# Kernel tuning notes

Measured on AMD Instinct MI355X. Metric: run time of the kernel, lower is better.

Reference implementation:

```python
import jax, jax.numpy as jnp
import numpy as np

E = 1408      # hidden_size
H = 16        # num heads
D = E // H    # head_dim = 88
S = 1025      # (448/14)^2 + 1 cls token
B = 8


def setup_inputs() -> dict:
    key = jax.random.key(0)
    ks = jax.random.split(key, 11)
    scale = 1.0 / np.sqrt(E)
    inp = {
        "hidden_states": jax.random.normal(ks[0], (B, S, E), dtype=jnp.float32),
    }
    # rotary freqs as cos/sin of random angles, shape (S, D//2)
    theta = jax.random.uniform(ks[1], (S, D // 2), dtype=jnp.float32) * (2.0 * np.pi)
    inp["freqs_cos"] = jnp.cos(theta)
    inp["freqs_sin"] = jnp.sin(theta)
    # projection weights stored torch-style: (out_features, in_features)
    inp["q_w"] = jax.random.normal(ks[2], (E, E), dtype=jnp.float32) * scale
    inp["q_b"] = jax.random.normal(ks[3], (E,), dtype=jnp.float32) * scale
    inp["k_w"] = jax.random.normal(ks[4], (E, E), dtype=jnp.float32) * scale
    inp["k_b"] = jax.random.normal(ks[5], (E,), dtype=jnp.float32) * scale
    inp["v_w"] = jax.random.normal(ks[6], (E, E), dtype=jnp.float32) * scale
    inp["v_b"] = jax.random.normal(ks[7], (E,), dtype=jnp.float32) * scale
    inp["o_w"] = jax.random.normal(ks[8], (E, E), dtype=jnp.float32) * scale
    inp["o_b"] = jax.random.normal(ks[9], (E,), dtype=jnp.float32) * scale
    return inp


def _apply_rope(x, cos, sin):
    # x: (B, S, H, D); interpret last dim as D//2 complex pairs (re, im)
    xr = x.astype(jnp.float32).reshape(*x.shape[:-1], D // 2, 2)
    re, im = xr[..., 0], xr[..., 1]
    c = cos[None, :, None, :]  # broadcast over batch and heads
    s = sin[None, :, None, :]
    out_re = re * c - im * s
    out_im = re * s + im * c
    return jnp.stack([out_re, out_im], axis=-1).reshape(x.shape).astype(x.dtype)


def reference(hidden_states, freqs_cos, freqs_sin, q_w, q_b, k_w, k_b, v_w, v_b, o_w, o_b):
    b, s, _ = hidden_states.shape
    q = (hidden_states @ q_w.T + q_b).reshape(b, s, H, D)
    k = (hidden_states @ k_w.T + k_b).reshape(b, s, H, D)
    v = (hidden_states @ v_w.T + v_b).reshape(b, s, H, D)
    q = _apply_rope(q, freqs_cos, freqs_sin)
    k = _apply_rope(k, freqs_cos, freqs_sin)
    # (B, H, S, D)
    q = q.transpose(0, 2, 1, 3)
    k = k.transpose(0, 2, 1, 3)
    v = v.transpose(0, 2, 1, 3)
    scores = jnp.einsum('bhqd,bhkd->bhqk', q, k) / np.sqrt(D)
    attn = jax.nn.softmax(scores.astype(jnp.float32), axis=-1).astype(q.dtype)
    out = jnp.einsum('bhqk,bhkd->bqhd', attn, v).reshape(b, s, H * D)
    out = out @ o_w.T + o_b
    return out, attn
```

## Files before the change

kernel.cpp:

```cpp
#include <hip/hip_runtime.h>

typedef unsigned short u16;
typedef __attribute__((ext_vector_type(8))) short short8;
typedef __attribute__((ext_vector_type(4))) float f32x4;
typedef __attribute__((ext_vector_type(16))) float f32x16;

#define E_DIM 1408
#define H_HEADS 16
#define S_SEQ 1025
#define B_BATCH 8
#define S_PAD 1088
#define D_PAD 128
#define M_ROWS 8200
#define M_PAD 8320

struct __attribute__((packed, aligned(4))) f4u { float x, y, z, w; };

__device__ __forceinline__ u16 f2bf(float f){
  union { float f; unsigned u; } x; x.f = f;
  unsigned r = x.u + 0x7fffu + ((x.u >> 16) & 1u);
  return (u16)(r >> 16);
}

__device__ __forceinline__ void gload16(const void* g, void* l){
  __builtin_amdgcn_global_load_lds(
      (const __attribute__((address_space(1))) void*)g,
      (__attribute__((address_space(3))) void*)l, 16, 0, 0);
}

__device__ __forceinline__ f32x4 mfma16(short8 a, short8 b, f32x4 c){
  return __builtin_amdgcn_mfma_f32_16x16x32_bf16(a, b, c, 0, 0, 0);
}
__device__ __forceinline__ f32x16 mfma32(short8 a, short8 b, f32x16 c){
  return __builtin_amdgcn_mfma_f32_32x32x16_bf16(a, b, c, 0, 0, 0);
}

__global__ __launch_bounds__(256) void cvt_kernel(const float* __restrict__ src,
                                                  u16* __restrict__ dst, int n8){
  int i = blockIdx.x * 256 + threadIdx.x;
  if (i >= n8) return;
  const float4* s4 = (const float4*)src;
  float4 a = s4[2*i], b = s4[2*i+1];
  union { u16 u[8]; short8 v; } o;
  o.u[0]=f2bf(a.x); o.u[1]=f2bf(a.y); o.u[2]=f2bf(a.z); o.u[3]=f2bf(a.w);
  o.u[4]=f2bf(b.x); o.u[5]=f2bf(b.y); o.u[6]=f2bf(b.z); o.u[7]=f2bf(b.w);
  ((short8*)dst)[i] = o.v;
}

__global__ __launch_bounds__(256) void zero_pads_kernel(u16* __restrict__ Q,
                                                        u16* __restrict__ K,
                                                        u16* __restrict__ Vt){
  int i = blockIdx.x * 256 + threadIdx.x;
  const int n1 = 128 * S_PAD * 8;
  const int n2 = 128 * 63 * 96;
  const int n3 = 128 * 96 * 63;
  if (i < n1){
    int d = 88 + (i & 7); int t = i >> 3;
    int s = t % S_PAD; int bh = t / S_PAD;
    size_t o = ((size_t)bh * S_PAD + s) * D_PAD + d;
    Q[o] = 0; K[o] = 0;
  } else if (i < n1 + n2){
    int j = i - n1;
    int d = j % 96; int t = j / 96;
    int s = 1025 + t % 63; int bh = t / 63;
    size_t o = ((size_t)bh * S_PAD + s) * D_PAD + d;
    Q[o] = 0; K[o] = 0;
  } else if (i < n1 + n2 + n3){
    int j = i - n1 - n2;
    int d = j % 96; int t = j / 96;
    int sp = 1025 + t % 63; int bh = t / 63;
    Vt[((size_t)bh * D_PAD + d) * S_PAD + sp] = 0;
  }
}

template<int MODE>
__global__ __launch_bounds__(256) void gemm_bt(
    const u16* __restrict__ A, const u16* __restrict__ W,
    const float* __restrict__ b_q, const float* __restrict__ b_k,
    const float* __restrict__ b_v,
    u16* __restrict__ Qb, u16* __restrict__ Kb, u16* __restrict__ Vtb,
    float* __restrict__ outF,
    const float* __restrict__ fcos, const float* __restrict__ fsin)
{
  __shared__ u16 As[128*32];
  __shared__ u16 Bs[128*32];
  const int tid = threadIdx.x;
  const int lane = tid & 63, wid = tid >> 6;
  const int cl = lane & 15, grp = lane >> 4;
  const int n0 = blockIdx.x * 128, m0 = blockIdx.y * 128;
  const int region = (MODE == 0) ? (blockIdx.x / 11) : 0;
  const int wm = (wid >> 1) * 64, wn = (wid & 1) * 64;
  f32x4 acc[4][4] = {};

  for (int k0 = 0; k0 < E_DIM; k0 += 32){
    __syncthreads();
#pragma unroll
    for (int rd = 0; rd < 2; ++rd){
      int G = rd * 256 + tid;
      int row = G >> 2, cg = G & 3;
      gload16(A + (size_t)(m0 + row) * E_DIM + k0 + cg * 8, (char*)As + (size_t)G * 16);
      gload16(W + (size_t)(n0 + row) * E_DIM + k0 + cg * 8, (char*)Bs + (size_t)G * 16);
    }
    __syncthreads();
    short8 av[4], bv[4];
#pragma unroll
    for (int i = 0; i < 4; ++i) av[i] = *(const short8*)&As[(wm + i*16 + cl)*32 + grp*8];
#pragma unroll
    for (int j = 0; j < 4; ++j) bv[j] = *(const short8*)&Bs[(wn + j*16 + cl)*32 + grp*8];
#pragma unroll
    for (int i = 0; i < 4; ++i)
#pragma unroll
      for (int j = 0; j < 4; ++j)
        acc[i][j] = mfma16(av[i], bv[j], acc[i][j]);
  }

  const float* bias = (MODE == 1) ? b_q : (region == 0 ? b_q : (region == 1 ? b_k : b_v));

#pragma unroll
  for (int i = 0; i < 4; ++i){
#pragma unroll
    for (int j = 0; j < 4; ++j){
      const int jcol = n0 + wn + j*16 + cl;
      const int jl = jcol - region * E_DIM;
      const float bsv = bias[jl];
      const int hh = jl / 88;
      const int dd = jl - hh * 88;
#pragma unroll
      for (int r = 0; r < 4; ++r){
        const int rrow = m0 + wm + i*16 + grp*4 + r;
        float v = acc[i][j][r] + bsv;
        if (MODE == 0 && region <= 1){
          float other = __shfl_xor(v, 1);
          int bb = rrow / 1025;
          int spos = rrow - bb * 1025;
          int pp = dd >> 1;
          float c = fcos[spos * 44 + pp];
          float s = fsin[spos * 44 + pp];
          float o = fmaf(v, c, (jl & 1) ? (other * s) : -(other * s));
          if (rrow < M_ROWS){
            size_t dst = (((size_t)(bb * 16 + hh)) * S_PAD + spos) * D_PAD + dd;
            (region ? Kb : Qb)[dst] = f2bf(o);
          }
        } else if (MODE == 0){
          if (rrow < M_ROWS){
            int bb = rrow / 1025;
            int spos = rrow - bb * 1025;
            size_t dst = (((size_t)(bb * 16 + hh)) * D_PAD + dd) * S_PAD + spos;
            Vtb[dst] = f2bf(v);
          }
        } else {
          if (rrow < M_ROWS) outF[(size_t)rrow * E_DIM + jcol] = v;
        }
      }
    }
  }
}

#define STAGE_K(buf, kt)                                                        \
  {                                                                             \
    _Pragma("unroll")                                                           \
    for (int rd = 0; rd < 2; ++rd){                                             \
      int G = rd * 512 + tid;                                                   \
      int row = G >> 4, c = G & 15;                                             \
      gload16(Kg + (size_t)((kt) * 64 + row) * 128 + ((c ^ (row & 15)) * 8),    \
              (char*)&Ks[buf][0] + (size_t)G * 16);                             \
    }                                                                           \
  }

#define STAGE_V(buf, kt)                                                        \
  {                                                                             \
    { int G = tid; int row = G >> 3, c = G & 7;                                 \
      gload16(Vg + (size_t)row * S_PAD + (kt) * 64 + ((c ^ (row & 7)) * 8),     \
              (char*)&Vs[buf][0] + (size_t)G * 16); }                           \
    if (tid < 256){                                                             \
      int G = 512 + tid; int row = G >> 3, c = G & 7;                           \
      gload16(Vg + (size_t)row * S_PAD + (kt) * 64 + ((c ^ (row & 7)) * 8),     \
              (char*)&Vs[buf][0] + (size_t)G * 16); }                           \
  }

__global__ __launch_bounds__(512) void attn_kernel(
    const u16* __restrict__ Qb, const u16* __restrict__ Kb,
    const u16* __restrict__ Vtb, float* __restrict__ attn,
    u16* __restrict__ AO)
{
  __shared__ u16 Ks[2][64 * 128];
  __shared__ u16 Vs[2][96 * 64];
  const int tid = threadIdx.x, wid = tid >> 6, lane = tid & 63;
  const int q5 = lane & 31, hi = lane >> 5;
  int lin = blockIdx.x + gridDim.x * blockIdx.y;
  lin = (lin & 7) * 80 + (lin >> 3);
  const int qt = lin % 5, bh = lin / 5;
  const int b = bh >> 4, h = bh & 15;
  const u16* __restrict__ Qg = Qb + (size_t)bh * S_PAD * 128;
  const u16* __restrict__ Kg = Kb + (size_t)bh * S_PAD * 128;
  const u16* __restrict__ Vg = Vtb + (size_t)bh * 128 * S_PAD;
  const int qrow = qt * 256 + wid * 32 + q5;
  const int qrowc = (qrow < S_PAD) ? qrow : (S_PAD - 1);
  const float SCALE = 0.10660035817780521f;

  short8 qf[6];
#pragma unroll
  for (int ds = 0; ds < 6; ++ds)
    qf[ds] = *(const short8*)&Qg[(size_t)qrowc * 128 + ds * 16 + hi * 8];

  float l_run = 0.f;
  STAGE_K(0, 0);
  __syncthreads();
  for (int kt = 0; kt < 17; ++kt){
    const int cur = kt & 1;
    if (kt < 16) STAGE_K(cur ^ 1, kt + 1);
#pragma unroll
    for (int ks = 0; ks < 2; ++ks){
      f32x16 sc = {};
      const int krow = ks * 32 + q5;
#pragma unroll
      for (int ds = 0; ds < 6; ++ds){
        int c = ds * 2 + hi;
        short8 kf = *(const short8*)&Ks[cur][krow * 128 + ((c ^ (krow & 15)) * 8)];
        sc = mfma32(kf, qf[ds], sc);
      }
      if (kt == 16){
#pragma unroll
        for (int r = 0; r < 16; ++r){
          int kabs = 1024 + ks * 32 + (r & 3) + 8 * (r >> 2) + 4 * hi;
          l_run += (kabs < 1025) ? __expf(sc[r] * SCALE) : 0.f;
        }
      } else {
#pragma unroll
        for (int r = 0; r < 16; ++r) l_run += __expf(sc[r] * SCALE);
      }
    }
    __syncthreads();
  }
  l_run += __shfl_xor(l_run, 32);
  const float linv = 1.0f / l_run;

  f32x16 oacc[3] = {};
  STAGE_K(0, 0);
  STAGE_V(0, 0);
  __syncthreads();
  for (int kt = 0; kt < 17; ++kt){
    const int cur = kt & 1;
    if (kt < 16){ STAGE_K(cur ^ 1, kt + 1); STAGE_V(cur ^ 1, kt + 1); }
#pragma unroll
    for (int ks = 0; ks < 2; ++ks){
      f32x16 sc = {};
      const int krow = ks * 32 + q5;
#pragma unroll
      for (int ds = 0; ds < 6; ++ds){
        int c = ds * 2 + hi;
        short8 kf = *(const short8*)&Ks[cur][krow * 128 + ((c ^ (krow & 15)) * 8)];
        sc = mfma32(kf, qf[ds], sc);
      }
#pragma unroll
      for (int r = 0; r < 16; ++r) sc[r] = __expf(sc[r] * SCALE) * linv;

      if (qrow < 1025){
        if (kt < 16){
          float* arow = attn + ((size_t)bh * 1025 + qrow) * 1025 + kt * 64 + ks * 32 + 4 * hi;
#pragma unroll
          for (int g = 0; g < 4; ++g){
            f4u w4 = { sc[4*g], sc[4*g+1], sc[4*g+2], sc[4*g+3] };
            *(f4u*)(arow + 8 * g) = w4;
          }
        } else {
#pragma unroll
          for (int r = 0; r < 16; ++r){
            int kabs = 1024 + ks * 32 + (r & 3) + 8 * (r >> 2) + 4 * hi;
            if (kabs < 1025)
              attn[((size_t)bh * 1025 + qrow) * 1025 + kabs] = sc[r];
          }
        }
      }

      unsigned w[8], sx[8];
#pragma unroll
      for (int j = 0; j < 8; ++j)
        w[j] = (unsigned)f2bf(sc[2*j]) | ((unsigned)f2bf(sc[2*j+1]) << 16);
#pragma unroll
      for (int j = 0; j < 8; ++j) sx[j] = __shfl_xor(w[j], 32);
      union U { unsigned u[4]; short8 s8; } a0, a1;
      a0.u[0] = hi ? sx[2] : w[0];
      a0.u[1] = hi ? sx[3] : w[1];
      a0.u[2] = hi ? w[2]  : sx[0];
      a0.u[3] = hi ? w[3]  : sx[1];
      a1.u[0] = hi ? sx[6] : w[4];
      a1.u[1] = hi ? sx[7] : w[5];
      a1.u[2] = hi ? w[6]  : sx[4];
      a1.u[3] = hi ? w[7]  : sx[5];

#pragma unroll
      for (int dt = 0; dt < 3; ++dt){
        const int vrow = dt * 32 + q5;
        int c0 = ks * 4 + hi;
        short8 vf0 = *(const short8*)&Vs[cur][vrow * 64 + ((c0 ^ (vrow & 7)) * 8)];
        oacc[dt] = mfma32(a0.s8, vf0, oacc[dt]);
        int c1 = ks * 4 + 2 + hi;
        short8 vf1 = *(const short8*)&Vs[cur][vrow * 64 + ((c1 ^ (vrow & 7)) * 8)];
        oacc[dt] = mfma32(a1.s8, vf1, oacc[dt]);
      }
    }
    __syncthreads();
  }

  const int qb0 = qt * 256 + wid * 32;
#pragma unroll
  for (int dt = 0; dt < 3; ++dt){
    const int d = dt * 32 + q5;
    if (d < 88){
#pragma unroll
      for (int r = 0; r < 16; ++r){
        int qq = qb0 + (r & 3) + 8 * (r >> 2) + 4 * hi;
        if (qq < 1025)
          AO[((size_t)b * 1025 + qq) * E_DIM + h * 88 + d] = f2bf(oacc[dt][r]);
      }
    }
  }
}

extern "C" void kernel_launch(void* const* d_in, const int* in_sizes, int n_in,
                              void* d_out, int out_size, void* d_ws, size_t ws_size,
                              hipStream_t stream)
{
  const float* hs   = (const float*)d_in[0];
  const float* fcos = (const float*)d_in[1];
  const float* fsin = (const float*)d_in[2];
  const float* q_w  = (const float*)d_in[3];
  const float* q_b  = (const float*)d_in[4];
  const float* k_w  = (const float*)d_in[5];
  const float* k_b  = (const float*)d_in[6];
  const float* v_w  = (const float*)d_in[7];
  const float* v_b  = (const float*)d_in[8];
  const float* o_w  = (const float*)d_in[9];
  const float* o_b  = (const float*)d_in[10];
  float* out0 = (float*)d_out;
  float* attn = out0 + (size_t)B_BATCH * S_SEQ * E_DIM;

  char* ws = (char*)d_ws;
  size_t off = 0;
  auto take = [&](size_t bytes){
    char* p = ws + off; off += (bytes + 255) & ~(size_t)255; return p;
  };
  u16* Xb  = (u16*)take((size_t)M_PAD * E_DIM * 2);
  u16* Wb  = (u16*)take((size_t)4 * E_DIM * E_DIM * 2);
  u16* Qb  = (u16*)take((size_t)128 * S_PAD * D_PAD * 2);
  u16* Kb  = (u16*)take((size_t)128 * S_PAD * D_PAD * 2);
  u16* Vtb = (u16*)take((size_t)128 * D_PAD * S_PAD * 2);
  u16* AO  = (u16*)take((size_t)M_PAD * E_DIM * 2);

  cvt_kernel<<<(1443200 + 255) / 256, 256, 0, stream>>>(hs, Xb, 1443200);
  cvt_kernel<<<968, 256, 0, stream>>>(q_w, Wb + 0 * (size_t)E_DIM * E_DIM, 247808);
  cvt_kernel<<<968, 256, 0, stream>>>(k_w, Wb + 1 * (size_t)E_DIM * E_DIM, 247808);
  cvt_kernel<<<968, 256, 0, stream>>>(v_w, Wb + 2 * (size_t)E_DIM * E_DIM, 247808);
  cvt_kernel<<<968, 256, 0, stream>>>(o_w, Wb + 3 * (size_t)E_DIM * E_DIM, 247808);
  zero_pads_kernel<<<10400, 256, 0, stream>>>(Qb, Kb, Vtb);

  gemm_bt<0><<<dim3(33, 65), 256, 0, stream>>>(Xb, Wb, q_b, k_b, v_b,
                                               Qb, Kb, Vtb, nullptr, fcos, fsin);

  attn_kernel<<<dim3(5, 128), 512, 0, stream>>>(Qb, Kb, Vtb, attn, AO);

  gemm_bt<1><<<dim3(11, 65), 256, 0, stream>>>(AO, Wb + 3 * (size_t)E_DIM * E_DIM,
                                               o_b, o_b, o_b,
                                               nullptr, nullptr, nullptr, out0, fcos, fsin);
}
```

Baseline: 587.2 us.

## Restructure attention tiling, fold softmax scale into Q, batch weight conversions

Several changes land at once. The softmax scale times log2(e) is folded into Q inside the QKV GEMM epilogue, so attention can use exp2 directly and apply the normaliser as a log subtraction. The attention kernel moves to 128-query blocks with 256 threads and a single V buffer, and uses cvt_pk_bf16 plus permlane32_swap for the P repack. The GEMM gets an XCD-aware block remap and s_setprio around its MFMAs, and the four weight conversions are merged into one launch. The padded-key correction subtracts a constant 63 (exp2(0) for each zero-padded key) instead of masking, which relies on padded K being exactly zero, and the single V buffer adds a synchronisation per tile.

```diff
diff --git a/kernel.cpp b/kernel.cpp
--- a/kernel.cpp
+++ b/kernel.cpp
@@ -33,6 +33,15 @@
 }
 __device__ __forceinline__ f32x16 mfma32(short8 a, short8 b, f32x16 c){
   return __builtin_amdgcn_mfma_f32_32x32x16_bf16(a, b, c, 0, 0, 0);
+}
+
+__device__ __forceinline__ unsigned cvtpk(float a, float b){
+  unsigned r;
+  asm("v_cvt_pk_bf16_f32 %0, %1, %2" : "=v"(r) : "v"(a), "v"(b));
+  return r;
+}
+__device__ __forceinline__ void plswap(unsigned &a, unsigned &b){
+  asm("v_permlane32_swap_b32 %0, %1" : "+v"(a), "+v"(b));
 }
 
 __global__ __launch_bounds__(256) void cvt_kernel(const float* __restrict__ src,
@@ -45,6 +54,24 @@
   o.u[0]=f2bf(a.x); o.u[1]=f2bf(a.y); o.u[2]=f2bf(a.z); o.u[3]=f2bf(a.w);
   o.u[4]=f2bf(b.x); o.u[5]=f2bf(b.y); o.u[6]=f2bf(b.z); o.u[7]=f2bf(b.w);
   ((short8*)dst)[i] = o.v;
+}
+
+__global__ __launch_bounds__(256) void cvt4_kernel(const float* __restrict__ s0,
+                                                   const float* __restrict__ s1,
+                                                   const float* __restrict__ s2,
+                                                   const float* __restrict__ s3,
+                                                   u16* __restrict__ dst, int n8){
+  int i = blockIdx.x * 256 + threadIdx.x;
+  if (i >= n8) return;
+  const float* src = (blockIdx.y == 0) ? s0 : (blockIdx.y == 1) ? s1
+                   : (blockIdx.y == 2) ? s2 : s3;
+  u16* d = dst + (size_t)blockIdx.y * n8 * 8;
+  const float4* s4 = (const float4*)src;
+  float4 a = s4[2*i], b = s4[2*i+1];
+  union { u16 u[8]; short8 v; } o;
+  o.u[0]=f2bf(a.x); o.u[1]=f2bf(a.y); o.u[2]=f2bf(a.z); o.u[3]=f2bf(a.w);
+  o.u[4]=f2bf(b.x); o.u[5]=f2bf(b.y); o.u[6]=f2bf(b.z); o.u[7]=f2bf(b.w);
+  ((short8*)d)[i] = o.v;
 }
 
 __global__ __launch_bounds__(256) void zero_pads_kernel(u16* __restrict__ Q,
@@ -87,8 +114,16 @@
   const int tid = threadIdx.x;
   const int lane = tid & 63, wid = tid >> 6;
   const int cl = lane & 15, grp = lane >> 4;
-  const int n0 = blockIdx.x * 128, m0 = blockIdx.y * 128;
-  const int region = (MODE == 0) ? (blockIdx.x / 11) : 0;
+
+  const int nwg = (int)(gridDim.x * gridDim.y);
+  const int orig = blockIdx.x + gridDim.x * blockIdx.y;
+  const int qq = nwg >> 3, rr = nwg & 7;
+  const int xcd = orig & 7, kk = orig >> 3;
+  const int wg = (xcd < rr ? xcd * (qq + 1) : rr * (qq + 1) + (xcd - rr) * qq) + kk;
+  const int bx = wg % (int)gridDim.x, by = wg / (int)gridDim.x;
+
+  const int n0 = bx * 128, m0 = by * 128;
+  const int region = (MODE == 0) ? (bx / 11) : 0;
   const int wm = (wid >> 1) * 64, wn = (wid & 1) * 64;
   f32x4 acc[4][4] = {};
 
@@ -107,14 +142,17 @@
     for (int i = 0; i < 4; ++i) av[i] = *(const short8*)&As[(wm + i*16 + cl)*32 + grp*8];
 #pragma unroll
     for (int j = 0; j < 4; ++j) bv[j] = *(const short8*)&Bs[(wn + j*16 + cl)*32 + grp*8];
+    __builtin_amdgcn_s_setprio(1);
 #pragma unroll
     for (int i = 0; i < 4; ++i)
 #pragma unroll
       for (int j = 0; j < 4; ++j)
         acc[i][j] = mfma16(av[i], bv[j], acc[i][j]);
+    __builtin_amdgcn_s_setprio(0);
   }
 
   const float* bias = (MODE == 1) ? b_q : (region == 0 ? b_q : (region == 1 ? b_k : b_v));
+  const float QSCALE = 0.15379181f;
 
 #pragma unroll
   for (int i = 0; i < 4; ++i){
@@ -137,6 +175,7 @@
           float c = fcos[spos * 44 + pp];
           float s = fsin[spos * 44 + pp];
           float o = fmaf(v, c, (jl & 1) ? (other * s) : -(other * s));
+          if (region == 0) o *= QSCALE;
           if (rrow < M_ROWS){
             size_t dst = (((size_t)(bb * 16 + hh)) * S_PAD + spos) * D_PAD + dd;
             (region ? Kb : Qb)[dst] = f2bf(o);
@@ -159,51 +198,50 @@
 #define STAGE_K(buf, kt)                                                        \
   {                                                                             \
     _Pragma("unroll")                                                           \
-    for (int rd = 0; rd < 2; ++rd){                                             \
-      int G = rd * 512 + tid;                                                   \
+    for (int rd = 0; rd < 4; ++rd){                                             \
+      int G = rd * 256 + tid;                                                   \
       int row = G >> 4, c = G & 15;                                             \
       gload16(Kg + (size_t)((kt) * 64 + row) * 128 + ((c ^ (row & 15)) * 8),    \
               (char*)&Ks[buf][0] + (size_t)G * 16);                             \
     }                                                                           \
   }
 
-#define STAGE_V(buf, kt)                                                        \
+#define STAGE_V(kt)                                                             \
   {                                                                             \
-    { int G = tid; int row = G >> 3, c = G & 7;                                 \
+    _Pragma("unroll")                                                           \
+    for (int rd = 0; rd < 3; ++rd){                                             \
+      int G = rd * 256 + tid;                                                   \
+      int row = G >> 3, c = G & 7;                                              \
       gload16(Vg + (size_t)row * S_PAD + (kt) * 64 + ((c ^ (row & 7)) * 8),     \
-              (char*)&Vs[buf][0] + (size_t)G * 16); }                           \
-    if (tid < 256){                                                             \
-      int G = 512 + tid; int row = G >> 3, c = G & 7;                           \
-      gload16(Vg + (size_t)row * S_PAD + (kt) * 64 + ((c ^ (row & 7)) * 8),     \
-              (char*)&Vs[buf][0] + (size_t)G * 16); }                           \
-  }
-
-__global__ __launch_bounds__(512) void attn_kernel(
+              (char*)Vs + (size_t)G * 16);                                      \
+    }                                                                           \
+  }
+
+__global__ __launch_bounds__(256, 3) void attn_kernel(
     const u16* __restrict__ Qb, const u16* __restrict__ Kb,
     const u16* __restrict__ Vtb, float* __restrict__ attn,
     u16* __restrict__ AO)
 {
   __shared__ u16 Ks[2][64 * 128];
-  __shared__ u16 Vs[2][96 * 64];
+  __shared__ u16 Vs[96 * 64];
   const int tid = threadIdx.x, wid = tid >> 6, lane = tid & 63;
   const int q5 = lane & 31, hi = lane >> 5;
   int lin = blockIdx.x + gridDim.x * blockIdx.y;
-  lin = (lin & 7) * 80 + (lin >> 3);
-  const int qt = lin % 5, bh = lin / 5;
+  lin = (lin & 7) * 144 + (lin >> 3);
+  const int qt = lin % 9, bh = lin / 9;
   const int b = bh >> 4, h = bh & 15;
   const u16* __restrict__ Qg = Qb + (size_t)bh * S_PAD * 128;
   const u16* __restrict__ Kg = Kb + (size_t)bh * S_PAD * 128;
   const u16* __restrict__ Vg = Vtb + (size_t)bh * 128 * S_PAD;
-  const int qrow = qt * 256 + wid * 32 + q5;
+  const int qrow = qt * 128 + wid * 32 + q5;
   const int qrowc = (qrow < S_PAD) ? qrow : (S_PAD - 1);
-  const float SCALE = 0.10660035817780521f;
 
   short8 qf[6];
 #pragma unroll
   for (int ds = 0; ds < 6; ++ds)
     qf[ds] = *(const short8*)&Qg[(size_t)qrowc * 128 + ds * 16 + hi * 8];
 
-  float l_run = 0.f;
+  float l0 = 0.f, l1 = 0.f, l2 = 0.f, l3 = 0.f;
   STAGE_K(0, 0);
   __syncthreads();
   for (int kt = 0; kt < 17; ++kt){
@@ -213,47 +251,51 @@
     for (int ks = 0; ks < 2; ++ks){
       f32x16 sc = {};
       const int krow = ks * 32 + q5;
+      __builtin_amdgcn_s_setprio(1);
 #pragma unroll
       for (int ds = 0; ds < 6; ++ds){
         int c = ds * 2 + hi;
         short8 kf = *(const short8*)&Ks[cur][krow * 128 + ((c ^ (krow & 15)) * 8)];
         sc = mfma32(kf, qf[ds], sc);
       }
-      if (kt == 16){
-#pragma unroll
-        for (int r = 0; r < 16; ++r){
-          int kabs = 1024 + ks * 32 + (r & 3) + 8 * (r >> 2) + 4 * hi;
-          l_run += (kabs < 1025) ? __expf(sc[r] * SCALE) : 0.f;
-        }
-      } else {
-#pragma unroll
-        for (int r = 0; r < 16; ++r) l_run += __expf(sc[r] * SCALE);
+      __builtin_amdgcn_s_setprio(0);
+#pragma unroll
+      for (int r = 0; r < 16; r += 4){
+        l0 += __builtin_amdgcn_exp2f(sc[r]);
+        l1 += __builtin_amdgcn_exp2f(sc[r+1]);
+        l2 += __builtin_amdgcn_exp2f(sc[r+2]);
+        l3 += __builtin_amdgcn_exp2f(sc[r+3]);
       }
     }
     __syncthreads();
   }
-  l_run += __shfl_xor(l_run, 32);
-  const float linv = 1.0f / l_run;
+  float l = (l0 + l1) + (l2 + l3);
+  l += __shfl_xor(l, 32);
+  l -= 63.0f;
+  const float lg2l = __builtin_amdgcn_logf(l);
 
   f32x16 oacc[3] = {};
   STAGE_K(0, 0);
-  STAGE_V(0, 0);
+  STAGE_V(0);
   __syncthreads();
   for (int kt = 0; kt < 17; ++kt){
     const int cur = kt & 1;
-    if (kt < 16){ STAGE_K(cur ^ 1, kt + 1); STAGE_V(cur ^ 1, kt + 1); }
+    if (kt < 16) STAGE_K(cur ^ 1, kt + 1);
+    short8 pa0[2], pa1[2];
 #pragma unroll
     for (int ks = 0; ks < 2; ++ks){
       f32x16 sc = {};
       const int krow = ks * 32 + q5;
+      __builtin_amdgcn_s_setprio(1);
 #pragma unroll
       for (int ds = 0; ds < 6; ++ds){
         int c = ds * 2 + hi;
         short8 kf = *(const short8*)&Ks[cur][krow * 128 + ((c ^ (krow & 15)) * 8)];
         sc = mfma32(kf, qf[ds], sc);
       }
-#pragma unroll
-      for (int r = 0; r < 16; ++r) sc[r] = __expf(sc[r] * SCALE) * linv;
+      __builtin_amdgcn_s_setprio(0);
+#pragma unroll
+      for (int r = 0; r < 16; ++r) sc[r] = __builtin_amdgcn_exp2f(sc[r] - lg2l);
 
       if (qrow < 1025){
         if (kt < 16){
@@ -273,46 +315,47 @@
         }
       }
 
-      unsigned w[8], sx[8];
-#pragma unroll
-      for (int j = 0; j < 8; ++j)
-        w[j] = (unsigned)f2bf(sc[2*j]) | ((unsigned)f2bf(sc[2*j+1]) << 16);
-#pragma unroll
-      for (int j = 0; j < 8; ++j) sx[j] = __shfl_xor(w[j], 32);
-      union U { unsigned u[4]; short8 s8; } a0, a1;
-      a0.u[0] = hi ? sx[2] : w[0];
-      a0.u[1] = hi ? sx[3] : w[1];
-      a0.u[2] = hi ? w[2]  : sx[0];
-      a0.u[3] = hi ? w[3]  : sx[1];
-      a1.u[0] = hi ? sx[6] : w[4];
-      a1.u[1] = hi ? sx[7] : w[5];
-      a1.u[2] = hi ? w[6]  : sx[4];
-      a1.u[3] = hi ? w[7]  : sx[5];
-
+      unsigned w0 = cvtpk(sc[0],  sc[1]),  w1 = cvtpk(sc[2],  sc[3]);
+      unsigned w2 = cvtpk(sc[4],  sc[5]),  w3 = cvtpk(sc[6],  sc[7]);
+      unsigned w4 = cvtpk(sc[8],  sc[9]),  w5 = cvtpk(sc[10], sc[11]);
+      unsigned w6 = cvtpk(sc[12], sc[13]), w7 = cvtpk(sc[14], sc[15]);
+      plswap(w0, w2); plswap(w1, w3); plswap(w4, w6); plswap(w5, w7);
+      union U { unsigned u[4]; short8 s8; } A0, A1;
+      A0.u[0] = w0; A0.u[1] = w1; A0.u[2] = w2; A0.u[3] = w3;
+      A1.u[0] = w4; A1.u[1] = w5; A1.u[2] = w6; A1.u[3] = w7;
+      pa0[ks] = A0.s8; pa1[ks] = A1.s8;
+    }
+
+    __syncthreads();
+    __builtin_amdgcn_s_setprio(1);
+#pragma unroll
+    for (int ks = 0; ks < 2; ++ks){
 #pragma unroll
       for (int dt = 0; dt < 3; ++dt){
         const int vrow = dt * 32 + q5;
         int c0 = ks * 4 + hi;
-        short8 vf0 = *(const short8*)&Vs[cur][vrow * 64 + ((c0 ^ (vrow & 7)) * 8)];
-        oacc[dt] = mfma32(a0.s8, vf0, oacc[dt]);
+        short8 vf0 = *(const short8*)&Vs[vrow * 64 + ((c0 ^ (vrow & 7)) * 8)];
+        oacc[dt] = mfma32(pa0[ks], vf0, oacc[dt]);
         int c1 = ks * 4 + 2 + hi;
-        short8 vf1 = *(const short8*)&Vs[cur][vrow * 64 + ((c1 ^ (vrow & 7)) * 8)];
-        oacc[dt] = mfma32(a1.s8, vf1, oacc[dt]);
-      }
-    }
+        short8 vf1 = *(const short8*)&Vs[vrow * 64 + ((c1 ^ (vrow & 7)) * 8)];
+        oacc[dt] = mfma32(pa1[ks], vf1, oacc[dt]);
+      }
+    }
+    __builtin_amdgcn_s_setprio(0);
     __syncthreads();
-  }
-
-  const int qb0 = qt * 256 + wid * 32;
+    if (kt < 16) STAGE_V(kt + 1);
+  }
+
+  const int qb0 = qt * 128 + wid * 32;
 #pragma unroll
   for (int dt = 0; dt < 3; ++dt){
     const int d = dt * 32 + q5;
     if (d < 88){
 #pragma unroll
       for (int r = 0; r < 16; ++r){
-        int qq = qb0 + (r & 3) + 8 * (r >> 2) + 4 * hi;
-        if (qq < 1025)
-          AO[((size_t)b * 1025 + qq) * E_DIM + h * 88 + d] = f2bf(oacc[dt][r]);
+        int qq2 = qb0 + (r & 3) + 8 * (r >> 2) + 4 * hi;
+        if (qq2 < 1025)
+          AO[((size_t)b * 1025 + qq2) * E_DIM + h * 88 + d] = f2bf(oacc[dt][r]);
       }
     }
   }
@@ -349,16 +392,13 @@
   u16* AO  = (u16*)take((size_t)M_PAD * E_DIM * 2);
 
   cvt_kernel<<<(1443200 + 255) / 256, 256, 0, stream>>>(hs, Xb, 1443200);
-  cvt_kernel<<<968, 256, 0, stream>>>(q_w, Wb + 0 * (size_t)E_DIM * E_DIM, 247808);
-  cvt_kernel<<<968, 256, 0, stream>>>(k_w, Wb + 1 * (size_t)E_DIM * E_DIM, 247808);
-  cvt_kernel<<<968, 256, 0, stream>>>(v_w, Wb + 2 * (size_t)E_DIM * E_DIM, 247808);
-  cvt_kernel<<<968, 256, 0, stream>>>(o_w, Wb + 3 * (size_t)E_DIM * E_DIM, 247808);
+  cvt4_kernel<<<dim3(968, 4), 256, 0, stream>>>(q_w, k_w, v_w, o_w, Wb, 247808);
   zero_pads_kernel<<<10400, 256, 0, stream>>>(Qb, Kb, Vtb);
 
   gemm_bt<0><<<dim3(33, 65), 256, 0, stream>>>(Xb, Wb, q_b, k_b, v_b,
                                                Qb, Kb, Vtb, nullptr, fcos, fsin);
 
-  attn_kernel<<<dim3(5, 128), 512, 0, stream>>>(Qb, Kb, Vtb, attn, AO);
+  attn_kernel<<<dim3(9, 128), 256, 0, stream>>>(Qb, Kb, Vtb, attn, AO);
 
   gemm_bt<1><<<dim3(11, 65), 256, 0, stream>>>(AO, Wb + 3 * (size_t)E_DIM * E_DIM,
                                                o_b, o_b, o_b,
```

Measured after the change: 547.9 us. -6.7%, faster.
